# Performance work log

Measured on AMD Instinct MI355X. Metric: run time of the kernel, lower is better.

## Reference

```python
import jax, jax.numpy as jnp
import numpy as np

# --- static Cayley table for Cl(3) (8 blades) ---
def _derive_cayley_table():
    basis_gens = [(), (1,), (2,), (3,), (1, 2), (1, 3), (2, 3), (1, 2, 3)]
    gens_to_idx = {g: i for i, g in enumerate(basis_gens)}
    def reduce(a, b):
        gens = list(a) + list(b)
        sign = 1
        changed = True
        while changed:
            changed = False
            i = 0
            while i < len(gens) - 1:
                if gens[i] == gens[i + 1]:
                    gens.pop(i); gens.pop(i)
                    changed = True
                    if i > 0:
                        i -= 1
                elif gens[i] > gens[i + 1]:
                    gens[i], gens[i + 1] = gens[i + 1], gens[i]
                    sign *= -1
                    changed = True
                    i += 1
                else:
                    i += 1
        return gens_to_idx[tuple(gens)], sign
    return [[reduce(basis_gens[i], basis_gens[j]) for j in range(8)] for i in range(8)]

_TAB = _derive_cayley_table()
SI = np.array([i for i in range(8) for _ in range(8)], dtype=np.int32)
SJ = np.array([j for _ in range(8) for j in range(8)], dtype=np.int32)
TK = np.array([_TAB[i][j][0] for i in range(8) for j in range(8)], dtype=np.int32)
SG = np.array([float(_TAB[i][j][1]) for i in range(8) for j in range(8)], dtype=np.float32)

N_TOK, N_BLADE, D_BLADE, D_FFN = 8192, 8, 256, 1024
LN_EPS = 1e-5


def setup_inputs() -> dict:
    key = jax.random.key(0)
    ks = jax.random.split(key, 5)
    scale = 0.02
    return {
        'x': jax.random.normal(ks[0], (N_TOK, N_BLADE, D_BLADE), jnp.float32),
        'interaction_weights': jnp.full((64,), 0.1, jnp.float32),
        'geo_gate': jnp.asarray(0.5, jnp.float32),
        'ln_w': jnp.ones((D_BLADE,), jnp.float32),
        'ln_b': jnp.zeros((D_BLADE,), jnp.float32),
        'W_gate': jax.random.normal(ks[1], (D_BLADE, D_FFN), jnp.float32) * scale,
        'W_up': jax.random.normal(ks[2], (D_BLADE, D_FFN), jnp.float32) * scale,
        'W_down': jax.random.normal(ks[3], (D_FFN, D_BLADE), jnp.float32) * scale,
    }


def reference(x, interaction_weights, geo_gate, ln_w, ln_b, W_gate, W_up, W_down):
    si = jnp.asarray(SI); sj = jnp.asarray(SJ); tk = jnp.asarray(TK)
    sg = jnp.asarray(SG).astype(x.dtype)
    w = jax.nn.sigmoid(interaction_weights).astype(x.dtype)
    # gather blade pairs, weighted Cayley product: (N, 64, D)
    products = x[:, si, :] * x[:, sj, :] * (sg * w)[None, :, None]
    # scatter-add into target blades: (N, 8, D)
    geo = jnp.zeros_like(x).at[:, tk, :].add(products)
    g = jax.nn.sigmoid(geo_gate)
    mixed = g * geo + (1.0 - g) * x
    # LayerNorm over D
    flat = mixed.reshape(-1, x.shape[-1])
    mu = jnp.mean(flat, axis=-1, keepdims=True)
    var = jnp.var(flat, axis=-1, keepdims=True)
    flat = (flat - mu) * jax.lax.rsqrt(var + LN_EPS) * ln_w + ln_b
    # SwiGLU FFN
    h = jax.nn.silu(flat @ W_gate) * (flat @ W_up)
    out = (h @ W_down).reshape(x.shape)
    return x + out
```

## Files before the change

kernel.cpp:

```cpp
#include <hip/hip_runtime.h>
#include <hip/hip_bf16.h>
#include <hip/hip_fp8.h>

typedef __bf16 bf16x8 __attribute__((ext_vector_type(8)));
typedef float floatx4 __attribute__((ext_vector_type(4)));
typedef float floatx16 __attribute__((ext_vector_type(16)));

constexpr int TK[64] = {
  0,1,2,3,4,5,6,7,
  1,0,4,5,2,3,7,6,
  2,4,0,6,1,7,3,5,
  3,5,6,0,7,1,2,4,
  4,2,1,7,0,6,5,3,
  5,3,7,1,6,0,4,2,
  6,7,3,2,5,4,0,1,
  7,6,5,4,3,2,1,0
};
constexpr float SGN[64] = {
  1, 1, 1, 1, 1, 1, 1, 1,
  1, 1, 1, 1, 1, 1, 1, 1,
  1,-1, 1, 1,-1,-1, 1,-1,
  1,-1,-1, 1, 1,-1,-1, 1,
  1,-1, 1, 1,-1,-1, 1,-1,
  1,-1,-1, 1, 1,-1,-1, 1,
  1, 1,-1, 1,-1, 1,-1,-1,
  1, 1,-1, 1,-1, 1,-1,-1
};

__device__ __forceinline__ void async16(const void* g, void* l) {
  __builtin_amdgcn_global_load_lds(
      (const __attribute__((address_space(1))) void*)g,
      (__attribute__((address_space(3))) void*)l, 16, 0, 0);
}

__device__ __forceinline__ unsigned char to_fp8(float v) {
  __hip_fp8_e4m3 q(v);
  return (unsigned char)q.__x;
}

__global__ __launch_bounds__(256) void transpose_cast(
    const float* __restrict__ src, __bf16* __restrict__ dst, int K, int N)
{
  __shared__ float s[32 * 33];
  const int t = threadIdx.x;
  const int k0 = blockIdx.y * 32, n0 = blockIdx.x * 32;
  const int r = t >> 5, c = t & 31;
  #pragma unroll
  for (int i = 0; i < 4; ++i)
    s[(r + i * 8) * 33 + c] = src[(size_t)(k0 + r + i * 8) * N + n0 + c];
  __syncthreads();
  #pragma unroll
  for (int i = 0; i < 4; ++i)
    dst[(size_t)(n0 + r + i * 8) * K + k0 + c] = (__bf16)s[c * 33 + r + i * 8];
}

__global__ __launch_bounds__(256) void transpose_cast_fp8(
    const float* __restrict__ src, unsigned char* __restrict__ dst, int K, int N)
{
  __shared__ float s[32 * 33];
  const int t = threadIdx.x;
  const int k0 = blockIdx.y * 32, n0 = blockIdx.x * 32;
  const int r = t >> 5, c = t & 31;
  #pragma unroll
  for (int i = 0; i < 4; ++i)
    s[(r + i * 8) * 33 + c] = src[(size_t)(k0 + r + i * 8) * N + n0 + c];
  __syncthreads();
  #pragma unroll
  for (int i = 0; i < 4; ++i)
    dst[(size_t)(n0 + r + i * 8) * K + k0 + c] = to_fp8(16.f * s[c * 33 + r + i * 8]);
}

__global__ __launch_bounds__(256) void geo_ln(
    const float* __restrict__ X,
    const float* __restrict__ IW,
    const float* __restrict__ GG,
    const float* __restrict__ LW, const float* __restrict__ LB,
    __bf16* __restrict__ F)
{
  __shared__ float sw[64];
  __shared__ float smix[8 * 256];
  __shared__ float sstat[16];
  const int t = threadIdx.x;
  const int tok = blockIdx.x;

  if (t < 64) sw[t] = SGN[t] / (1.f + __expf(-IW[t]));

  float xv[8];
  #pragma unroll
  for (int b = 0; b < 8; ++b) xv[b] = X[(size_t)tok * 2048 + b * 256 + t];
  const float g = 1.f / (1.f + __expf(-GG[0]));

  __syncthreads();

  float geo[8] = {0.f, 0.f, 0.f, 0.f, 0.f, 0.f, 0.f, 0.f};
  #pragma unroll
  for (int p = 0; p < 64; ++p)
    geo[TK[p]] += xv[p >> 3] * xv[p & 7] * sw[p];

  float mv[8];
  #pragma unroll
  for (int b = 0; b < 8; ++b) {
    mv[b] = g * geo[b] + (1.f - g) * xv[b];
    smix[b * 256 + t] = mv[b];
  }
  __syncthreads();

  const int wv = t >> 6, lane = t & 63;
  #pragma unroll
  for (int s = 0; s < 2; ++s) {
    int b = wv * 2 + s;
    float v0 = smix[b * 256 + lane];
    float v1 = smix[b * 256 + 64 + lane];
    float v2 = smix[b * 256 + 128 + lane];
    float v3 = smix[b * 256 + 192 + lane];
    float sum = v0 + v1 + v2 + v3;
    float sq  = v0*v0 + v1*v1 + v2*v2 + v3*v3;
    #pragma unroll
    for (int off = 32; off > 0; off >>= 1) {
      sum += __shfl_xor(sum, off, 64);
      sq  += __shfl_xor(sq,  off, 64);
    }
    if (lane == 0) {
      float mu  = sum * (1.f / 256.f);
      float var = sq * (1.f / 256.f) - mu * mu;
      sstat[b]     = mu;
      sstat[8 + b] = rsqrtf(var + 1e-5f);
    }
  }
  __syncthreads();

  const float lw = LW[t], lb = LB[t];
  #pragma unroll
  for (int b = 0; b < 8; ++b) {
    float v = (mv[b] - sstat[b]) * sstat[8 + b] * lw + lb;
    F[(size_t)(tok * 8 + b) * 256 + t] = (__bf16)v;
  }
}

__global__ __launch_bounds__(256, 3) void gemm_gateup(
    const __bf16* __restrict__ A,
    const __bf16* __restrict__ Bg,
    const __bf16* __restrict__ Bu,
    unsigned char* __restrict__ H)
{
  __shared__ __align__(16) char smem[32768];
  __bf16* sA  = (__bf16*)smem;
  __bf16* sBg = (__bf16*)(smem + 16384);
  __bf16* sBu = (__bf16*)(smem + 24576);
  unsigned char* sH = (unsigned char*)(smem + 16384);

  const int t = threadIdx.x;
  const int f0 = blockIdx.x * 64;
  const int m0 = blockIdx.y * 128;
  const int lane = t & 63, wv = t >> 6;
  const int wm = wv & 1, wf = wv >> 1;
  const int l31 = lane & 31, half = lane >> 5;

  int aoff[4], boff[2];
  #pragma unroll
  for (int i = 0; i < 4; ++i) {
    int idx = i * 256 + t, row = idx >> 3, slot = idx & 7;
    aoff[i] = (m0 + row) * 256 + (slot ^ (row & 7)) * 8;
  }
  #pragma unroll
  for (int i = 0; i < 2; ++i) {
    int idx = i * 256 + t, row = idx >> 3, slot = idx & 7;
    boff[i] = (f0 + row) * 256 + (slot ^ (row & 7)) * 8;
  }

  floatx16 accg[2], accu[2];
  #pragma unroll
  for (int i = 0; i < 2; ++i)
    #pragma unroll
    for (int r = 0; r < 16; ++r) { accg[i][r] = 0.f; accu[i][r] = 0.f; }

  const int xr = l31 & 7;
  const int rowA0 = (wm * 64 + l31) * 64;
  const int rowA1 = rowA0 + 32 * 64;
  const int rowB  = (wf * 32 + l31) * 64;

  for (int k = 0; k < 4; ++k) {
    const int kk = k * 64;
    #pragma unroll
    for (int i = 0; i < 4; ++i) async16(A + aoff[i] + kk, &sA[(i * 256 + t) * 8]);
    #pragma unroll
    for (int i = 0; i < 2; ++i) {
      async16(Bg + boff[i] + kk, &sBg[(i * 256 + t) * 8]);
      async16(Bu + boff[i] + kk, &sBu[(i * 256 + t) * 8]);
    }
    __syncthreads();

    #pragma unroll
    for (int s = 0; s < 4; ++s) {
      const int oct = ((s * 2 + half) ^ xr) * 8;
      bf16x8 a0 = *(const bf16x8*)&sA[rowA0 + oct];
      bf16x8 a1 = *(const bf16x8*)&sA[rowA1 + oct];
      bf16x8 bg = *(const bf16x8*)&sBg[rowB + oct];
      bf16x8 bu = *(const bf16x8*)&sBu[rowB + oct];
      accg[0] = __builtin_amdgcn_mfma_f32_32x32x16_bf16(a0, bg, accg[0], 0, 0, 0);
      accu[0] = __builtin_amdgcn_mfma_f32_32x32x16_bf16(a0, bu, accu[0], 0, 0, 0);
      accg[1] = __builtin_amdgcn_mfma_f32_32x32x16_bf16(a1, bg, accg[1], 0, 0, 0);
      accu[1] = __builtin_amdgcn_mfma_f32_32x32x16_bf16(a1, bu, accu[1], 0, 0, 0);
    }
    __syncthreads();
  }

  #pragma unroll
  for (int i = 0; i < 2; ++i)
    #pragma unroll
    for (int r = 0; r < 16; ++r) {
      int crow = (r & 3) + 8 * (r >> 2) + 4 * half;
      int m_l = wm * 64 + i * 32 + crow;
      float gv = accg[i][r], uv = accu[i][r];
      float hv = (gv / (1.f + __expf(-gv))) * uv;
      sH[m_l * 64 + wf * 32 + l31] = to_fp8(16.f * hv);
    }
  __syncthreads();
  #pragma unroll
  for (int i = 0; i < 2; ++i) {
    int chunk = i * 256 + t;
    int m = chunk >> 2, c = chunk & 3;
    *(int4*)&H[(size_t)(m0 + m) * 1024 + f0 + c * 16] = *(const int4*)&sH[m * 64 + c * 16];
  }
}

__global__ __launch_bounds__(256, 2) void gemm_down(
    const unsigned char* __restrict__ A,
    const unsigned char* __restrict__ B,
    const float* __restrict__ X,
    float* __restrict__ O)
{
  __shared__ unsigned char sA[128 * 64];
  __shared__ unsigned char sB[256 * 64];
  const int t = threadIdx.x;
  const int m0 = blockIdx.x * 128;
  const int lane = t & 63, wv = t >> 6;
  const int wm = wv & 1, wn = wv >> 1;
  const int l15 = lane & 15, quad = lane >> 4;

  int aoff[2], boff[4];
  #pragma unroll
  for (int i = 0; i < 2; ++i) {
    int idx = i * 256 + t, row = idx >> 2, q = idx & 3;
    aoff[i] = (m0 + row) * 1024 + (q ^ ((row >> 1) & 3)) * 16;
  }
  #pragma unroll
  for (int i = 0; i < 4; ++i) {
    int idx = i * 256 + t, row = idx >> 2, q = idx & 3;
    boff[i] = row * 1024 + (q ^ ((row >> 1) & 3)) * 16;
  }

  floatx4 zero = {0.f, 0.f, 0.f, 0.f};
  floatx4 acc[4][8];
  #pragma unroll
  for (int i = 0; i < 4; ++i)
    #pragma unroll
    for (int j = 0; j < 8; ++j) acc[i][j] = zero;

  int aaddr[2][4], baddr[2][8];
  #pragma unroll
  for (int s = 0; s < 2; ++s) {
    const int u = s * 4 + quad;
    #pragma unroll
    for (int i = 0; i < 4; ++i) {
      int r = wm * 64 + i * 16 + l15;
      aaddr[s][i] = r * 64 + (((u >> 1) ^ ((r >> 1) & 3)) << 4) + (u & 1) * 8;
    }
    #pragma unroll
    for (int j = 0; j < 8; ++j) {
      int r = wn * 128 + j * 16 + l15;
      baddr[s][j] = r * 64 + (((u >> 1) ^ ((r >> 1) & 3)) << 4) + (u & 1) * 8;
    }
  }

  for (int k = 0; k < 16; ++k) {
    const int kk = k * 64;
    #pragma unroll
    for (int i = 0; i < 2; ++i) async16(A + aoff[i] + kk, &sA[(i * 256 + t) * 16]);
    #pragma unroll
    for (int i = 0; i < 4; ++i) async16(B + boff[i] + kk, &sB[(i * 256 + t) * 16]);
    __syncthreads();

    #pragma unroll
    for (int s = 0; s < 2; ++s) {
      long av[4], bv[8];
      #pragma unroll
      for (int i = 0; i < 4; ++i) av[i] = *(const long*)&sA[aaddr[s][i]];
      #pragma unroll
      for (int j = 0; j < 8; ++j) bv[j] = *(const long*)&sB[baddr[s][j]];
      #pragma unroll
      for (int i = 0; i < 4; ++i)
        #pragma unroll
        for (int j = 0; j < 8; ++j)
          acc[i][j] = __builtin_amdgcn_mfma_f32_16x16x32_fp8_fp8(av[i], bv[j], acc[i][j], 0, 0, 0);
    }
    __syncthreads();
  }

  #pragma unroll
  for (int i = 0; i < 4; ++i)
    #pragma unroll
    for (int j = 0; j < 8; ++j)
      #pragma unroll
      for (int r = 0; r < 4; ++r) {
        int m = m0 + wm * 64 + i * 16 + quad * 4 + r;
        int n = wn * 128 + j * 16 + l15;
        size_t o = (size_t)m * 256 + n;
        O[o] = X[o] + acc[i][j][r] * (1.f / 256.f);
      }
}

extern "C" void kernel_launch(void* const* d_in, const int* in_sizes, int n_in,
                              void* d_out, int out_size, void* d_ws, size_t ws_size,
                              hipStream_t stream) {
  const float* x   = (const float*)d_in[0];
  const float* iw  = (const float*)d_in[1];
  const float* gg  = (const float*)d_in[2];
  const float* lnw = (const float*)d_in[3];
  const float* lnb = (const float*)d_in[4];
  const float* Wg  = (const float*)d_in[5];
  const float* Wu  = (const float*)d_in[6];
  const float* Wd  = (const float*)d_in[7];
  float* out = (float*)d_out;

  char* ws = (char*)d_ws;
  __bf16*        flat = (__bf16*)(ws);
  unsigned char* h    = (unsigned char*)(ws + 33554432);
  __bf16*        Bg   = (__bf16*)(ws + 100663296);
  __bf16*        Bu   = (__bf16*)(ws + 101187584);
  unsigned char* Bd   = (unsigned char*)(ws + 101711872);

  transpose_cast<<<dim3(32, 8),  256, 0, stream>>>(Wg, Bg, 256, 1024);
  transpose_cast<<<dim3(32, 8),  256, 0, stream>>>(Wu, Bu, 256, 1024);
  transpose_cast_fp8<<<dim3(8, 32), 256, 0, stream>>>(Wd, Bd, 1024, 256);
  geo_ln<<<8192, 256, 0, stream>>>(x, iw, gg, lnw, lnb, flat);
  gemm_gateup<<<dim3(16, 512), 256, 0, stream>>>(flat, Bg, Bu, h);
  gemm_down<<<512, 256, 0, stream>>>(h, Bd, x, out);
}
```

Before: 285.8 us.

## Rewrite gate/up GEMM with 256x256 tiles, interleaved weights, and pipelined async loads

```diff
diff --git a/kernel.cpp b/kernel.cpp
--- a/kernel.cpp
+++ b/kernel.cpp
@@ -4,7 +4,6 @@
 
 typedef __bf16 bf16x8 __attribute__((ext_vector_type(8)));
 typedef float floatx4 __attribute__((ext_vector_type(4)));
-typedef float floatx16 __attribute__((ext_vector_type(16)));
 
 constexpr int TK[64] = {
   0,1,2,3,4,5,6,7,
@@ -38,20 +37,23 @@
   return (unsigned char)q.__x;
 }
 
-__global__ __launch_bounds__(256) void transpose_cast(
-    const float* __restrict__ src, __bf16* __restrict__ dst, int K, int N)
+__global__ __launch_bounds__(256) void transpose_cast_gu(
+    const float* __restrict__ src, __bf16* __restrict__ dst, int sel)
 {
   __shared__ float s[32 * 33];
   const int t = threadIdx.x;
-  const int k0 = blockIdx.y * 32, n0 = blockIdx.x * 32;
+  const int k0 = blockIdx.y * 32, f0 = blockIdx.x * 32;
   const int r = t >> 5, c = t & 31;
   #pragma unroll
   for (int i = 0; i < 4; ++i)
-    s[(r + i * 8) * 33 + c] = src[(size_t)(k0 + r + i * 8) * N + n0 + c];
-  __syncthreads();
-  #pragma unroll
-  for (int i = 0; i < 4; ++i)
-    dst[(size_t)(n0 + r + i * 8) * K + k0 + c] = (__bf16)s[c * 33 + r + i * 8];
+    s[(r + i * 8) * 33 + c] = src[(size_t)(k0 + r + i * 8) * 1024 + f0 + c];
+  __syncthreads();
+  #pragma unroll
+  for (int i = 0; i < 4; ++i) {
+    int f = f0 + r + i * 8;
+    int n = ((f >> 5) << 6) + sel * 32 + (f & 31);
+    dst[(size_t)n * 256 + k0 + c] = (__bf16)s[c * 33 + r + i * 8];
+  }
 }
 
 __global__ __launch_bounds__(256) void transpose_cast_fp8(
@@ -137,91 +139,163 @@
   }
 }
 
-__global__ __launch_bounds__(256, 3) void gemm_gateup(
+__global__ __launch_bounds__(512, 2) void gemm_gateup(
     const __bf16* __restrict__ A,
-    const __bf16* __restrict__ Bg,
-    const __bf16* __restrict__ Bu,
+    const __bf16* __restrict__ B,
     unsigned char* __restrict__ H)
 {
-  __shared__ __align__(16) char smem[32768];
-  __bf16* sA  = (__bf16*)smem;
-  __bf16* sBg = (__bf16*)(smem + 16384);
-  __bf16* sBu = (__bf16*)(smem + 24576);
-  unsigned char* sH = (unsigned char*)(smem + 16384);
+  __shared__ __align__(16) char smc[65536];
 
   const int t = threadIdx.x;
-  const int f0 = blockIdx.x * 64;
-  const int m0 = blockIdx.y * 128;
-  const int lane = t & 63, wv = t >> 6;
-  const int wm = wv & 1, wf = wv >> 1;
-  const int l31 = lane & 31, half = lane >> 5;
-
-  int aoff[4], boff[2];
-  #pragma unroll
-  for (int i = 0; i < 4; ++i) {
-    int idx = i * 256 + t, row = idx >> 3, slot = idx & 7;
-    aoff[i] = (m0 + row) * 256 + (slot ^ (row & 7)) * 8;
-  }
-  #pragma unroll
-  for (int i = 0; i < 2; ++i) {
-    int idx = i * 256 + t, row = idx >> 3, slot = idx & 7;
-    boff[i] = (f0 + row) * 256 + (slot ^ (row & 7)) * 8;
-  }
-
-  floatx16 accg[2], accu[2];
-  #pragma unroll
-  for (int i = 0; i < 2; ++i)
-    #pragma unroll
-    for (int r = 0; r < 16; ++r) { accg[i][r] = 0.f; accu[i][r] = 0.f; }
-
-  const int xr = l31 & 7;
-  const int rowA0 = (wm * 64 + l31) * 64;
-  const int rowA1 = rowA0 + 32 * 64;
-  const int rowB  = (wf * 32 + l31) * 64;
-
-  for (int k = 0; k < 4; ++k) {
-    const int kk = k * 64;
-    #pragma unroll
-    for (int i = 0; i < 4; ++i) async16(A + aoff[i] + kk, &sA[(i * 256 + t) * 8]);
-    #pragma unroll
-    for (int i = 0; i < 2; ++i) {
-      async16(Bg + boff[i] + kk, &sBg[(i * 256 + t) * 8]);
-      async16(Bu + boff[i] + kk, &sBu[(i * 256 + t) * 8]);
-    }
-    __syncthreads();
-
-    #pragma unroll
-    for (int s = 0; s < 4; ++s) {
-      const int oct = ((s * 2 + half) ^ xr) * 8;
-      bf16x8 a0 = *(const bf16x8*)&sA[rowA0 + oct];
-      bf16x8 a1 = *(const bf16x8*)&sA[rowA1 + oct];
-      bf16x8 bg = *(const bf16x8*)&sBg[rowB + oct];
-      bf16x8 bu = *(const bf16x8*)&sBu[rowB + oct];
-      accg[0] = __builtin_amdgcn_mfma_f32_32x32x16_bf16(a0, bg, accg[0], 0, 0, 0);
-      accu[0] = __builtin_amdgcn_mfma_f32_32x32x16_bf16(a0, bu, accu[0], 0, 0, 0);
-      accg[1] = __builtin_amdgcn_mfma_f32_32x32x16_bf16(a1, bg, accg[1], 0, 0, 0);
-      accu[1] = __builtin_amdgcn_mfma_f32_32x32x16_bf16(a1, bu, accu[1], 0, 0, 0);
-    }
-    __syncthreads();
-  }
-
-  #pragma unroll
-  for (int i = 0; i < 2; ++i)
-    #pragma unroll
-    for (int r = 0; r < 16; ++r) {
-      int crow = (r & 3) + 8 * (r >> 2) + 4 * half;
-      int m_l = wm * 64 + i * 32 + crow;
-      float gv = accg[i][r], uv = accu[i][r];
-      float hv = (gv / (1.f + __expf(-gv))) * uv;
-      sH[m_l * 64 + wf * 32 + l31] = to_fp8(16.f * hv);
-    }
-  __syncthreads();
-  #pragma unroll
-  for (int i = 0; i < 2; ++i) {
-    int chunk = i * 256 + t;
-    int m = chunk >> 2, c = chunk & 3;
-    *(int4*)&H[(size_t)(m0 + m) * 1024 + f0 + c * 16] = *(const int4*)&sH[m * 64 + c * 16];
-  }
+  const int l = t & 63;
+  const int wv = t >> 6, wm = wv & 1, wn = wv >> 1;
+  const int j4 = l >> 4;
+
+  const int bid = blockIdx.x;
+  const int lid = (bid & 7) * 256 + (bid >> 3);
+  const int m0 = (lid >> 3) * 256;
+  const int n0 = (lid & 7) * 256;
+
+  const int rA = t >> 3;
+  const int rB = ((t >> 8) * 64) + ((t & 255) >> 3);
+  const int cs = ((t & 7) ^ ((t >> 3) & 7)) * 8;
+  const __bf16* gA = A + (size_t)(m0 + rA) * 256 + cs;
+  const __bf16* gB = B + (size_t)(n0 + rB) * 256 + cs;
+  char* dA = smc + t * 16;
+  char* dB = smc + 32768 + (t >> 8) * 4096 + t * 16;
+
+#define STAGE_AE(KT) { async16(gA + (KT), dA);                 async16(gA + 32768 + (KT), dA + 16384); }
+#define STAGE_AO(KT) { async16(gA + 16384 + (KT), dA + 8192);  async16(gA + 49152 + (KT), dA + 24576); }
+#define STAGE_BE(KT) { async16(gB + (KT), dB);                 async16(gB + 32768 + (KT), dB + 16384); }
+#define STAGE_BO(KT) { async16(gB + 8192 + (KT), dB + 4096);   async16(gB + 40960 + (KT), dB + 20480); }
+
+  const int rbA = (wm * 128 + (l & 15)) * 128;
+  const int rbB = 32768 + (wn * 64 + (l & 15)) * 128;
+  const int sw0 = (j4 ^ (l & 7)) * 16;
+  const int sw1 = ((4 + j4) ^ (l & 7)) * 16;
+  const char* pA0 = smc + rbA + sw0;
+  const char* pA1 = smc + rbA + sw1;
+  const char* pB0 = smc + rbB + sw0;
+  const char* pB1 = smc + rbB + sw1;
+
+  bf16x8 aE[4][2], aO[4][2], bE[2][2], bO[2][2];
+  floatx4 acc[8][4];
+  #pragma unroll
+  for (int i = 0; i < 8; ++i)
+    #pragma unroll
+    for (int j = 0; j < 4; ++j)
+      acc[i][j] = floatx4{0.f, 0.f, 0.f, 0.f};
+
+#define MFMA_QUAD(av, bv, mo, no)                                         \
+  _Pragma("unroll")                                                       \
+  for (int kk = 0; kk < 2; ++kk)                                          \
+    _Pragma("unroll")                                                     \
+    for (int mi = 0; mi < 4; ++mi)                                        \
+      _Pragma("unroll")                                                   \
+      for (int nj = 0; nj < 2; ++nj)                                      \
+        acc[(mo) + mi][(no) + nj] = __builtin_amdgcn_mfma_f32_16x16x32_bf16( \
+            av[mi][kk], bv[nj][kk], acc[(mo) + mi][(no) + nj], 0, 0, 0);
+
+#define PHASE_MID()                                          \
+  __builtin_amdgcn_s_barrier();                              \
+  asm volatile("s_waitcnt lgkmcnt(0)" ::: "memory");         \
+  __builtin_amdgcn_sched_barrier(0);                         \
+  __builtin_amdgcn_s_setprio(1);
+
+#define PHASE_TAIL()                                         \
+  __builtin_amdgcn_s_setprio(0);                             \
+  __builtin_amdgcn_sched_barrier(0);
+
+  STAGE_AE(0); STAGE_BE(0); STAGE_BO(0); STAGE_AO(0);
+  asm volatile("s_waitcnt vmcnt(4)" ::: "memory");
+  __builtin_amdgcn_s_barrier();
+
+  #pragma unroll
+  for (int kt = 0; kt < 4; ++kt) {
+    const int ktn = (kt + 1) * 64;
+
+    #pragma unroll
+    for (int mi = 0; mi < 4; ++mi) {
+      aE[mi][0] = *(const bf16x8*)(pA0 + mi * 2048);
+      aE[mi][1] = *(const bf16x8*)(pA1 + mi * 2048);
+    }
+    #pragma unroll
+    for (int nj = 0; nj < 2; ++nj) {
+      bE[nj][0] = *(const bf16x8*)(pB0 + nj * 2048);
+      bE[nj][1] = *(const bf16x8*)(pB1 + nj * 2048);
+    }
+    PHASE_MID();
+    MFMA_QUAD(aE, bE, 0, 0);
+    PHASE_TAIL();
+    asm volatile("s_waitcnt vmcnt(2)" ::: "memory");
+    __builtin_amdgcn_s_barrier();
+
+    #pragma unroll
+    for (int nj = 0; nj < 2; ++nj) {
+      bO[nj][0] = *(const bf16x8*)(pB0 + 4096 + nj * 2048);
+      bO[nj][1] = *(const bf16x8*)(pB1 + 4096 + nj * 2048);
+    }
+    if (kt < 3) { STAGE_AE(ktn); STAGE_BE(ktn); }
+    PHASE_MID();
+    MFMA_QUAD(aE, bO, 0, 2);
+    PHASE_TAIL();
+    if (kt < 3) { asm volatile("s_waitcnt vmcnt(4)" ::: "memory"); }
+    else        { asm volatile("s_waitcnt vmcnt(0)" ::: "memory"); }
+    __builtin_amdgcn_s_barrier();
+
+    #pragma unroll
+    for (int mi = 0; mi < 4; ++mi) {
+      aO[mi][0] = *(const bf16x8*)(pA0 + 8192 + mi * 2048);
+      aO[mi][1] = *(const bf16x8*)(pA1 + 8192 + mi * 2048);
+    }
+    if (kt < 3) STAGE_BO(ktn);
+    PHASE_MID();
+    MFMA_QUAD(aO, bE, 4, 0);
+    PHASE_TAIL();
+    __builtin_amdgcn_s_barrier();
+
+    if (kt < 3) STAGE_AO(ktn);
+    PHASE_MID();
+    MFMA_QUAD(aO, bO, 4, 2);
+    PHASE_TAIL();
+    if (kt < 3) {
+      asm volatile("s_waitcnt vmcnt(4)" ::: "memory");
+      __builtin_amdgcn_s_barrier();
+    }
+  }
+
+  __syncthreads();
+  unsigned char* sH = (unsigned char*)smc;
+  #pragma unroll
+  for (int mi = 0; mi < 8; ++mi)
+    #pragma unroll
+    for (int nj = 0; nj < 2; ++nj) {
+      floatx4 gv4 = acc[mi][nj], uv4 = acc[mi][nj + 2];
+      int fcol = wn * 32 + nj * 16 + (l & 15);
+      #pragma unroll
+      for (int r = 0; r < 4; ++r) {
+        int mloc = wm * 128 + mi * 16 + j4 * 4 + r;
+        float gvv = gv4[r], uvv = uv4[r];
+        float hv = (gvv / (1.f + __expf(-gvv))) * uvv;
+        sH[mloc * 128 + fcol] = to_fp8(16.f * hv);
+      }
+    }
+  __syncthreads();
+  const size_t hbase = (size_t)m0 * 1024 + (n0 >> 1);
+  #pragma unroll
+  for (int c = 0; c < 4; ++c) {
+    int chunk = c * 512 + t;
+    int mloc = chunk >> 3, col = chunk & 7;
+    *(int4*)&H[hbase + (size_t)mloc * 1024 + col * 16] =
+        *(const int4*)&sH[mloc * 128 + col * 16];
+  }
+#undef STAGE_AE
+#undef STAGE_AO
+#undef STAGE_BE
+#undef STAGE_BO
+#undef MFMA_QUAD
+#undef PHASE_MID
+#undef PHASE_TAIL
 }
 
 __global__ __launch_bounds__(256, 2) void gemm_down(
@@ -326,14 +400,13 @@
   char* ws = (char*)d_ws;
   __bf16*        flat = (__bf16*)(ws);
   unsigned char* h    = (unsigned char*)(ws + 33554432);
-  __bf16*        Bg   = (__bf16*)(ws + 100663296);
-  __bf16*        Bu   = (__bf16*)(ws + 101187584);
+  __bf16*        Bil  = (__bf16*)(ws + 100663296);
   unsigned char* Bd   = (unsigned char*)(ws + 101711872);
 
-  transpose_cast<<<dim3(32, 8),  256, 0, stream>>>(Wg, Bg, 256, 1024);
-  transpose_cast<<<dim3(32, 8),  256, 0, stream>>>(Wu, Bu, 256, 1024);
+  transpose_cast_gu<<<dim3(32, 8), 256, 0, stream>>>(Wg, Bil, 0);
+  transpose_cast_gu<<<dim3(32, 8), 256, 0, stream>>>(Wu, Bil, 1);
   transpose_cast_fp8<<<dim3(8, 32), 256, 0, stream>>>(Wd, Bd, 1024, 256);
   geo_ln<<<8192, 256, 0, stream>>>(x, iw, gg, lnw, lnb, flat);
-  gemm_gateup<<<dim3(16, 512), 256, 0, stream>>>(flat, Bg, Bu, h);
+  gemm_gateup<<<2048, 512, 0, stream>>>(flat, Bil, h);
   gemm_down<<<512, 256, 0, stream>>>(h, Bd, x, out);
 }
```

Result: no change. 281.7 us (-1.4%).

## Remap gate/up GEMM blocks, extra LDS swizzle, transposed MFMA packed FP8 epilogue

Applied to the files above, without the earlier changes.

```diff
diff --git a/kernel.cpp b/kernel.cpp
--- a/kernel.cpp
+++ b/kernel.cpp
@@ -147,11 +147,13 @@
   __bf16* sA  = (__bf16*)smem;
   __bf16* sBg = (__bf16*)(smem + 16384);
   __bf16* sBu = (__bf16*)(smem + 24576);
-  unsigned char* sH = (unsigned char*)(smem + 16384);
-
-  const int t = threadIdx.x;
-  const int f0 = blockIdx.x * 64;
-  const int m0 = blockIdx.y * 128;
+  int* sD = (int*)(smem + 16384);
+
+  const int t = threadIdx.x;
+  const int bid = blockIdx.y * 16 + blockIdx.x;
+  const int lid = (bid & 7) * 1024 + (bid >> 3);
+  const int f0 = (lid & 15) * 64;
+  const int m0 = (lid >> 4) * 128;
   const int lane = t & 63, wv = t >> 6;
   const int wm = wv & 1, wf = wv >> 1;
   const int l31 = lane & 31, half = lane >> 5;
@@ -160,12 +162,12 @@
   #pragma unroll
   for (int i = 0; i < 4; ++i) {
     int idx = i * 256 + t, row = idx >> 3, slot = idx & 7;
-    aoff[i] = (m0 + row) * 256 + (slot ^ (row & 7)) * 8;
+    aoff[i] = (m0 + row) * 256 + (slot ^ (row & 7) ^ ((row >> 3) & 3)) * 8;
   }
   #pragma unroll
   for (int i = 0; i < 2; ++i) {
     int idx = i * 256 + t, row = idx >> 3, slot = idx & 7;
-    boff[i] = (f0 + row) * 256 + (slot ^ (row & 7)) * 8;
+    boff[i] = (f0 + row) * 256 + (slot ^ (row & 7) ^ ((row >> 3) & 3)) * 8;
   }
 
   floatx16 accg[2], accu[2];
@@ -174,7 +176,7 @@
     #pragma unroll
     for (int r = 0; r < 16; ++r) { accg[i][r] = 0.f; accu[i][r] = 0.f; }
 
-  const int xr = l31 & 7;
+  const int xr = (l31 & 7) ^ ((l31 >> 3) & 3);
   const int rowA0 = (wm * 64 + l31) * 64;
   const int rowA1 = rowA0 + 32 * 64;
   const int rowB  = (wf * 32 + l31) * 64;
@@ -197,30 +199,41 @@
       bf16x8 a1 = *(const bf16x8*)&sA[rowA1 + oct];
       bf16x8 bg = *(const bf16x8*)&sBg[rowB + oct];
       bf16x8 bu = *(const bf16x8*)&sBu[rowB + oct];
-      accg[0] = __builtin_amdgcn_mfma_f32_32x32x16_bf16(a0, bg, accg[0], 0, 0, 0);
-      accu[0] = __builtin_amdgcn_mfma_f32_32x32x16_bf16(a0, bu, accu[0], 0, 0, 0);
-      accg[1] = __builtin_amdgcn_mfma_f32_32x32x16_bf16(a1, bg, accg[1], 0, 0, 0);
-      accu[1] = __builtin_amdgcn_mfma_f32_32x32x16_bf16(a1, bu, accu[1], 0, 0, 0);
+      accg[0] = __builtin_amdgcn_mfma_f32_32x32x16_bf16(bg, a0, accg[0], 0, 0, 0);
+      accu[0] = __builtin_amdgcn_mfma_f32_32x32x16_bf16(bu, a0, accu[0], 0, 0, 0);
+      accg[1] = __builtin_amdgcn_mfma_f32_32x32x16_bf16(bg, a1, accg[1], 0, 0, 0);
+      accu[1] = __builtin_amdgcn_mfma_f32_32x32x16_bf16(bu, a1, accu[1], 0, 0, 0);
     }
     __syncthreads();
   }
 
   #pragma unroll
-  for (int i = 0; i < 2; ++i)
-    #pragma unroll
-    for (int r = 0; r < 16; ++r) {
-      int crow = (r & 3) + 8 * (r >> 2) + 4 * half;
-      int m_l = wm * 64 + i * 32 + crow;
-      float gv = accg[i][r], uv = accu[i][r];
-      float hv = (gv / (1.f + __expf(-gv))) * uv;
-      sH[m_l * 64 + wf * 32 + l31] = to_fp8(16.f * hv);
-    }
-  __syncthreads();
-  #pragma unroll
   for (int i = 0; i < 2; ++i) {
-    int chunk = i * 256 + t;
-    int m = chunk >> 2, c = chunk & 3;
-    *(int4*)&H[(size_t)(m0 + m) * 1024 + f0 + c * 16] = *(const int4*)&sH[m * 64 + c * 16];
+    const int m_l = wm * 64 + i * 32 + l31;
+    #pragma unroll
+    for (int q = 0; q < 4; ++q) {
+      float hv[4];
+      #pragma unroll
+      for (int e = 0; e < 4; ++e) {
+        float gv = accg[i][q * 4 + e], uv = accu[i][q * 4 + e];
+        hv[e] = 16.f * (gv / (1.f + __expf(-gv))) * uv;
+      }
+      int w = __builtin_amdgcn_cvt_pk_fp8_f32(hv[0], hv[1], 0, false);
+      w = __builtin_amdgcn_cvt_pk_fp8_f32(hv[2], hv[3], w, true);
+      sD[m_l * 17 + wf * 8 + half + 2 * q] = w;
+    }
+  }
+  __syncthreads();
+  #pragma unroll
+  for (int c = 0; c < 2; ++c) {
+    int chunk = c * 256 + t;
+    int m = chunk >> 2, q4 = chunk & 3;
+    int4 v;
+    v.x = sD[m * 17 + q4 * 4 + 0];
+    v.y = sD[m * 17 + q4 * 4 + 1];
+    v.z = sD[m * 17 + q4 * 4 + 2];
+    v.w = sD[m * 17 + q4 * 4 + 3];
+    *(int4*)&H[(size_t)(m0 + m) * 1024 + f0 + q4 * 16] = v;
   }
 }
 
```

Measured after the change: 279.1 us. 1.02x faster.
